# Performance work log

Hardware: AMD Instinct MI355X
Metric: run time of the kernel (lower is better)

The kernel has to match this reference:

```python
import jax, jax.numpy as jnp
import numpy as np

B, N, F = 32, 1024, 7
HID, HID_GLO, MLP_H, OUT = 256, 8, 64, 8
THRESHOLD = 0.3


def setup_inputs() -> dict:
    key = jax.random.key(0)
    ks = jax.random.split(key, 16)
    def lin(k, fan_out, fan_in):
        # xavier-uniform-like init
        lim = (6.0 / (fan_in + fan_out)) ** 0.5
        return jax.random.uniform(k, (fan_out, fan_in), jnp.float32, -lim, lim)
    return {
        "x": jax.random.normal(ks[0], (B, N, F), jnp.float32),
        "W1": lin(ks[1], HID, 2),   "b1": jnp.zeros((HID,), jnp.float32),
        "W2": lin(ks[2], HID, HID), "b2": jnp.zeros((HID,), jnp.float32),
        "Wfc": lin(ks[3], HID, HID), "bfc": jnp.zeros((HID,), jnp.float32),
        "Wg": lin(ks[4], HID_GLO, 2), "bg": jnp.zeros((HID_GLO,), jnp.float32),
        "Wm0": lin(ks[5], MLP_H, N * F), "bm0": jnp.zeros((MLP_H,), jnp.float32),
        "Wm1": lin(ks[6], MLP_H, MLP_H), "bm1": jnp.zeros((MLP_H,), jnp.float32),
        "Wp": lin(ks[7], OUT, MLP_H + HID + HID_GLO), "bp": jnp.zeros((OUT,), jnp.float32),
    }


def reference(x, W1, b1, W2, b2, Wfc, bfc, Wg, bg, Wm0, bm0, Wm1, bm1, Wp, bp):
    # --- GCN branch (torch code detaches node features & adjacency) ---
    pts = jax.lax.stop_gradient(x[:, :, 1:3])                     # [B,N,2]
    diff = pts[:, :, None, :] - pts[:, None, :, :]                # [B,N,N,2]
    dist = jnp.sqrt(jnp.sum(diff * diff, axis=-1))                # [B,N,N]
    adj = (dist < THRESHOLD).astype(x.dtype)                      # [B,N,N]
    dinv = 1.0 / jnp.sqrt(jnp.sum(adj, axis=-1))                  # [B,N] (>=1, self-loop)
    nadj = dinv[:, :, None] * adj * dinv[:, None, :]              # D^-1/2 A D^-1/2
    h = jax.nn.relu(jnp.einsum('bij,bjd->bid', nadj, pts) @ W1.T + b1)   # [B,N,256]
    g = jnp.einsum('bij,bjh->bih', nadj, h) @ W2.T + b2                  # [B,N,256]
    gcn_en = jnp.mean(g, axis=1) @ Wfc.T + bfc                    # [B,256]

    # --- global branch (torch code uses .item() -> constants) ---
    v = jax.lax.stop_gradient(x[:, :, 1:5])                       # [B,N,4]
    avg_speed = jnp.mean(jnp.linalg.norm(v[:, :, 2:4], axis=-1), axis=1)  # [B]
    density = 1.0 / jnp.max(dist, axis=(1, 2))                    # [B] (v3 == pts)
    glo_in = jnp.stack([avg_speed, density], axis=-1)             # [B,2]
    glo_en = jax.nn.relu(glo_in @ Wg.T + bg)                      # [B,8]

    # --- MLP branch on flattened x ---
    xf = x.reshape(x.shape[0], -1)                                # [B, N*F]
    xf = jax.nn.relu(xf @ Wm0.T + bm0)
    xf = jax.nn.relu(xf @ Wm1.T + bm1)                            # [B,64]

    out = jnp.concatenate([xf, gcn_en, glo_en], axis=1) @ Wp.T + bp  # [B,8]
    return out
```

## Files before the change

kernel.cpp:

```cpp
#include <hip/hip_runtime.h>

#define BB 32
#define NN 1024
#define FF 7
#define HID 256
#define MLPH 64
#define OUTN 8
#define CATN (MLPH + HID + 8)

__device__ __forceinline__ float wave_sum(float v) {
#pragma unroll
    for (int m = 32; m >= 1; m >>= 1) v += __shfl_xor(v, m, 64);
    return v;
}
__device__ __forceinline__ float wave_max(float v) {
#pragma unroll
    for (int m = 32; m >= 1; m >>= 1) v = fmaxf(v, __shfl_xor(v, m, 64));
    return v;
}

__global__ __launch_bounds__(1024, 4) void kA(const float* __restrict__ x,
                                              const float* __restrict__ Wm0,
                                              const float* __restrict__ W2,
                                              const float* __restrict__ b2,
                                              const float* __restrict__ Wfc,
                                              const float* __restrict__ bfc,
                                              const float* __restrict__ Wp,
                                              float* __restrict__ deg,
                                              float* __restrict__ bmaxp,
                                              float* __restrict__ spd,
                                              float* __restrict__ mlp_p,
                                              float* __restrict__ E,
                                              float* __restrict__ cE) {
    __shared__ __align__(16) float l0[NN];
    __shared__ __align__(16) float l1[NN];
    __shared__ __align__(16) float s2[NN];
    __shared__ __align__(16) float s3[NN];
    __shared__ float wred[16];
    int blk = blockIdx.x, tid = threadIdx.x, lane = tid & 63, w = tid >> 6;
    if (blk < 256) {
        int b = blk >> 3, jg = blk & 7;
        const float* xb = x + b * (NN * FF);
        l0[tid] = xb[tid * FF + 1];
        l1[tid] = xb[tid * FF + 2];
        __syncthreads();
        int jA = jg * 128 + lane, jB = jA + 64;
        float pj0a = l0[jA], pj1a = l1[jA];
        float pj0b = l0[jB], pj1b = l1[jB];
        const float4* v0p = (const float4*)&l0[w * 64];
        const float4* v1p = (const float4*)&l1[w * 64];
        unsigned dA = 0u, dB = 0u;
        float mx = 0.f;
#pragma unroll 4
        for (int g = 0; g < 16; ++g) {
            float4 v0 = v0p[g], v1 = v1p[g];
            float dx, dy, d2a, d2b;
            dx = pj0a - v0.x; dy = pj1a - v1.x; d2a = fmaf(dy, dy, dx * dx);
            dx = pj0b - v0.x; dy = pj1b - v1.x; d2b = fmaf(dy, dy, dx * dx);
            dA += (d2a <= 0.09f); dB += (d2b <= 0.09f);
            mx = fmaxf(mx, fmaxf(d2a, d2b));
            dx = pj0a - v0.y; dy = pj1a - v1.y; d2a = fmaf(dy, dy, dx * dx);
            dx = pj0b - v0.y; dy = pj1b - v1.y; d2b = fmaf(dy, dy, dx * dx);
            dA += (d2a <= 0.09f); dB += (d2b <= 0.09f);
            mx = fmaxf(mx, fmaxf(d2a, d2b));
            dx = pj0a - v0.z; dy = pj1a - v1.z; d2a = fmaf(dy, dy, dx * dx);
            dx = pj0b - v0.z; dy = pj1b - v1.z; d2b = fmaf(dy, dy, dx * dx);
            dA += (d2a <= 0.09f); dB += (d2b <= 0.09f);
            mx = fmaxf(mx, fmaxf(d2a, d2b));
            dx = pj0a - v0.w; dy = pj1a - v1.w; d2a = fmaf(dy, dy, dx * dx);
            dx = pj0b - v0.w; dy = pj1b - v1.w; d2b = fmaf(dy, dy, dx * dx);
            dA += (d2a <= 0.09f); dB += (d2b <= 0.09f);
            mx = fmaxf(mx, fmaxf(d2a, d2b));
        }
        s2[tid] = (float)dA;
        s3[tid] = (float)dB;
        mx = wave_max(mx);
        if (lane == 0) wred[w] = mx;
        __syncthreads();
        if (tid < 64) {
            float s = 0.f;
#pragma unroll
            for (int kk = 0; kk < 16; ++kk) s += s2[kk * 64 + tid];
            deg[b * NN + jg * 128 + tid] = s;
        } else if (tid < 128) {
            int t = tid - 64;
            float s = 0.f;
#pragma unroll
            for (int kk = 0; kk < 16; ++kk) s += s3[kk * 64 + t];
            deg[b * NN + jg * 128 + 64 + t] = s;
        }
        if (tid == 0) {
            float m = wred[0];
#pragma unroll
            for (int i = 1; i < 16; ++i) m = fmaxf(m, wred[i]);
            bmaxp[b * 8 + jg] = m;
        }
        if (jg == 0) {
            float vx = xb[tid * FF + 3], vy = xb[tid * FF + 4];
            float sp = sqrtf(fmaf(vx, vx, vy * vy));
            sp = wave_sum(sp);
            __syncthreads();
            if (lane == 0) wred[w] = sp;
            __syncthreads();
            if (tid == 0) {
                float s = 0.f;
#pragma unroll
                for (int i = 0; i < 16; ++i) s += wred[i];
                spd[b] = s;
            }
        }
    } else if (blk < 384) {
        int gid = (blk - 256) * 16 + w;
        int b = gid >> 6, h = gid & 63;
        const float4* wr = (const float4*)(Wm0 + h * (NN * FF));
        const float4* xr = (const float4*)(x + b * (NN * FF));
        float4 a4 = {0.f, 0.f, 0.f, 0.f};
#pragma unroll 7
        for (int it = 0; it < 28; ++it) {
            float4 wv = wr[it * 64 + lane];
            float4 xv = xr[it * 64 + lane];
            a4.x = fmaf(wv.x, xv.x, a4.x);
            a4.y = fmaf(wv.y, xv.y, a4.y);
            a4.z = fmaf(wv.z, xv.z, a4.z);
            a4.w = fmaf(wv.w, xv.w, a4.w);
        }
        float s = (a4.x + a4.y) + (a4.z + a4.w);
        s = wave_sum(s);
        if (lane == 0) mlp_p[gid] = s;
    } else {
        int o = blk - 384;
        if (tid < HID) l0[tid] = Wp[o * CATN + MLPH + tid];
        __syncthreads();
        if (tid < HID) {
            float a = 0.f;
#pragma unroll 8
            for (int m = 0; m < HID; ++m) a = fmaf(l0[m], Wfc[m * HID + tid], a);
            l1[tid] = a;
            s2[tid] = l0[tid] * bfc[tid];
        }
        __syncthreads();
        if (tid < HID) {
            float e = 0.f;
#pragma unroll 8
            for (int k = 0; k < HID; ++k) e = fmaf(l1[k], W2[k * HID + tid], e);
            E[o * HID + tid] = e;
            float c = fmaf(l1[tid], b2[tid], s2[tid]);
            c = wave_sum(c);
            if (lane == 0) wred[w] = c;
        }
        __syncthreads();
        if (tid == 0) cE[o] = wred[0] + wred[1] + wred[2] + wred[3];
    }
}

__global__ __launch_bounds__(1024, 4) void kB(const float* __restrict__ x,
                                              const float* __restrict__ deg,
                                              float* __restrict__ q0,
                                              float* __restrict__ q1,
                                              float* __restrict__ wj) {
    __shared__ __align__(16) float l0[NN];
    __shared__ __align__(16) float l1[NN];
    __shared__ __align__(16) float di[NN];
    __shared__ __align__(16) float r0a[NN];
    __shared__ __align__(16) float r1a[NN];
    __shared__ __align__(16) float r2a[NN];
    __shared__ __align__(16) float r0b[NN];
    __shared__ __align__(16) float r1b[NN];
    __shared__ __align__(16) float r2b[NN];
    int blk = blockIdx.x, tid = threadIdx.x, lane = tid & 63, w = tid >> 6;
    int b = blk >> 3, jg = blk & 7;
    const float* xb = x + b * (NN * FF);
    l0[tid] = xb[tid * FF + 1];
    l1[tid] = xb[tid * FF + 2];
    di[tid] = 1.0f / sqrtf(deg[b * NN + tid]);
    __syncthreads();
    int jA = jg * 128 + lane, jB = jA + 64;
    float pj0a = l0[jA], pj1a = l1[jA];
    float pj0b = l0[jB], pj1b = l1[jB];
    const float4* v0p = (const float4*)&l0[w * 64];
    const float4* v1p = (const float4*)&l1[w * 64];
    const float4* vdp = (const float4*)&di[w * 64];
    float a0a = 0.f, a1a = 0.f, asa = 0.f;
    float a0b = 0.f, a1b = 0.f, asb = 0.f;
#pragma unroll 4
    for (int g = 0; g < 16; ++g) {
        float4 v0 = v0p[g], v1 = v1p[g], vd = vdp[g];
        float dx, dy, d2, t;
        dx = pj0a - v0.x; dy = pj1a - v1.x; d2 = fmaf(dy, dy, dx * dx);
        t = (d2 <= 0.09f) ? vd.x : 0.0f;
        a0a = fmaf(t, v0.x, a0a); a1a = fmaf(t, v1.x, a1a); asa += t;
        dx = pj0b - v0.x; dy = pj1b - v1.x; d2 = fmaf(dy, dy, dx * dx);
        t = (d2 <= 0.09f) ? vd.x : 0.0f;
        a0b = fmaf(t, v0.x, a0b); a1b = fmaf(t, v1.x, a1b); asb += t;
        dx = pj0a - v0.y; dy = pj1a - v1.y; d2 = fmaf(dy, dy, dx * dx);
        t = (d2 <= 0.09f) ? vd.y : 0.0f;
        a0a = fmaf(t, v0.y, a0a); a1a = fmaf(t, v1.y, a1a); asa += t;
        dx = pj0b - v0.y; dy = pj1b - v1.y; d2 = fmaf(dy, dy, dx * dx);
        t = (d2 <= 0.09f) ? vd.y : 0.0f;
        a0b = fmaf(t, v0.y, a0b); a1b = fmaf(t, v1.y, a1b); asb += t;
        dx = pj0a - v0.z; dy = pj1a - v1.z; d2 = fmaf(dy, dy, dx * dx);
        t = (d2 <= 0.09f) ? vd.z : 0.0f;
        a0a = fmaf(t, v0.z, a0a); a1a = fmaf(t, v1.z, a1a); asa += t;
        dx = pj0b - v0.z; dy = pj1b - v1.z; d2 = fmaf(dy, dy, dx * dx);
        t = (d2 <= 0.09f) ? vd.z : 0.0f;
        a0b = fmaf(t, v0.z, a0b); a1b = fmaf(t, v1.z, a1b); asb += t;
        dx = pj0a - v0.w; dy = pj1a - v1.w; d2 = fmaf(dy, dy, dx * dx);
        t = (d2 <= 0.09f) ? vd.w : 0.0f;
        a0a = fmaf(t, v0.w, a0a); a1a = fmaf(t, v1.w, a1a); asa += t;
        dx = pj0b - v0.w; dy = pj1b - v1.w; d2 = fmaf(dy, dy, dx * dx);
        t = (d2 <= 0.09f) ? vd.w : 0.0f;
        a0b = fmaf(t, v0.w, a0b); a1b = fmaf(t, v1.w, a1b); asb += t;
    }
    r0a[tid] = a0a; r1a[tid] = a1a; r2a[tid] = asa;
    r0b[tid] = a0b; r1b[tid] = a1b; r2b[tid] = asb;
    __syncthreads();
    if (tid < 128) {
        int t = tid & 63;
        const float* R0 = (tid < 64) ? r0a : r0b;
        const float* R1 = (tid < 64) ? r1a : r1b;
        const float* R2 = (tid < 64) ? r2a : r2b;
        int j = jg * 128 + ((tid < 64) ? 0 : 64) + t;
        float s0 = 0.f, s1 = 0.f, ss = 0.f;
#pragma unroll
        for (int kk = 0; kk < 16; ++kk) {
            s0 += R0[kk * 64 + t];
            s1 += R1[kk * 64 + t];
            ss += R2[kk * 64 + t];
        }
        float dj = di[j];
        q0[b * NN + j] = dj * s0;
        q1[b * NN + j] = dj * s1;
        wj[b * NN + j] = dj * ss * (1.0f / NN);
    }
}

__global__ __launch_bounds__(1024, 4) void kF(const float* __restrict__ q0,
                                              const float* __restrict__ q1,
                                              const float* __restrict__ wj,
                                              const float* __restrict__ W1,
                                              const float* __restrict__ b1,
                                              const float* __restrict__ Wg,
                                              const float* __restrict__ bg,
                                              const float* __restrict__ Wm1,
                                              const float* __restrict__ bm1,
                                              const float* __restrict__ Wp,
                                              const float* __restrict__ bp,
                                              const float* __restrict__ bm0,
                                              const float* __restrict__ mlp_p,
                                              const float* __restrict__ bmaxp,
                                              const float* __restrict__ spd,
                                              const float* __restrict__ E,
                                              const float* __restrict__ cE,
                                              float* __restrict__ out) {
    __shared__ __align__(16) float sq0[NN];
    __shared__ __align__(16) float sq1[NN];
    __shared__ __align__(16) float sw[NN];
    __shared__ __align__(16) float hpp[4][HID];
    __shared__ __align__(16) float hs[HID];
    __shared__ float sx1[MLPH];
    __shared__ float sxf2[MLPH];
    __shared__ float sglo[8];
    int b = blockIdx.x, tid = threadIdx.x;
    sq0[tid] = q0[b * NN + tid];
    sq1[tid] = q1[b * NN + tid];
    sw[tid]  = wj[b * NN + tid];
    if (tid >= 448 && tid < 512) {
        int h = tid - 448;
        sx1[h] = fmaxf(mlp_p[b * MLPH + h] + bm0[h], 0.f);
    }
    __syncthreads();
    {
        int h = tid & 255, jq = tid >> 8;
        float w10 = W1[h * 2], w11 = W1[h * 2 + 1], bb = b1[h];
        float acc = 0.f;
        const float4* q0v4 = (const float4*)&sq0[jq * 256];
        const float4* q1v4 = (const float4*)&sq1[jq * 256];
        const float4* wv4  = (const float4*)&sw[jq * 256];
#pragma unroll 4
        for (int g = 0; g < 64; ++g) {
            float4 q0v = q0v4[g], q1v = q1v4[g], wv = wv4[g];
            acc = fmaf(wv.x, fmaxf(fmaf(q1v.x, w11, fmaf(q0v.x, w10, bb)), 0.f), acc);
            acc = fmaf(wv.y, fmaxf(fmaf(q1v.y, w11, fmaf(q0v.y, w10, bb)), 0.f), acc);
            acc = fmaf(wv.z, fmaxf(fmaf(q1v.z, w11, fmaf(q0v.z, w10, bb)), 0.f), acc);
            acc = fmaf(wv.w, fmaxf(fmaf(q1v.w, w11, fmaf(q0v.w, w10, bb)), 0.f), acc);
        }
        hpp[jq][h] = acc;
    }
    __syncthreads();
    if (tid < HID) {
        hs[tid] = hpp[0][tid] + hpp[1][tid] + hpp[2][tid] + hpp[3][tid];
    } else if (tid < HID + MLPH) {
        int t = tid - HID;
        float a = bm1[t];
        const float* wv = Wm1 + t * MLPH;
#pragma unroll
        for (int k = 0; k < MLPH; ++k) a = fmaf(wv[k], sx1[k], a);
        sxf2[t] = fmaxf(a, 0.f);
    } else if (tid < HID + MLPH + 8) {
        int t = tid - HID - MLPH;
        float mx = 0.f;
#pragma unroll
        for (int g = 0; g < 8; ++g) mx = fmaxf(mx, bmaxp[b * 8 + g]);
        float avg  = spd[b] * (1.0f / NN);
        float dens = 1.0f / sqrtf(mx);
        sglo[t] = fmaxf(fmaf(Wg[t * 2], avg, fmaf(Wg[t * 2 + 1], dens, bg[t])), 0.f);
    }
    __syncthreads();
    if (tid < 512) {
        int o = tid >> 6, lane = tid & 63;
        const float* Eo = E + o * HID;
        float a = Eo[lane] * hs[lane];
        a = fmaf(Eo[lane + 64],  hs[lane + 64],  a);
        a = fmaf(Eo[lane + 128], hs[lane + 128], a);
        a = fmaf(Eo[lane + 192], hs[lane + 192], a);
        a = fmaf(Wp[o * CATN + lane], sxf2[lane], a);
        a = wave_sum(a);
        if (lane == 0) {
            const float* wg = Wp + o * CATN + MLPH + HID;
#pragma unroll
            for (int g = 0; g < 8; ++g) a = fmaf(wg[g], sglo[g], a);
            out[b * OUTN + o] = a + cE[o] + bp[o];
        }
    }
}

extern "C" void kernel_launch(void* const* d_in, const int* in_sizes, int n_in,
                              void* d_out, int out_size, void* d_ws, size_t ws_size,
                              hipStream_t stream) {
    const float* x   = (const float*)d_in[0];
    const float* W1  = (const float*)d_in[1];
    const float* b1  = (const float*)d_in[2];
    const float* W2  = (const float*)d_in[3];
    const float* b2  = (const float*)d_in[4];
    const float* Wfc = (const float*)d_in[5];
    const float* bfc = (const float*)d_in[6];
    const float* Wg  = (const float*)d_in[7];
    const float* bg  = (const float*)d_in[8];
    const float* Wm0 = (const float*)d_in[9];
    const float* bm0 = (const float*)d_in[10];
    const float* Wm1 = (const float*)d_in[11];
    const float* bm1 = (const float*)d_in[12];
    const float* Wp  = (const float*)d_in[13];
    const float* bp  = (const float*)d_in[14];
    float* out = (float*)d_out;
    float* ws  = (float*)d_ws;

    float* deg   = ws;
    float* q0    = ws + 32768;
    float* q1    = ws + 65536;
    float* wj    = ws + 98304;
    float* mlp_p = ws + 131072;
    float* bmaxp = ws + 133120;
    float* spd   = ws + 133376;
    float* E     = ws + 133408;
    float* cE    = ws + 135456;

    kA<<<392, 1024, 0, stream>>>(x, Wm0, W2, b2, Wfc, bfc, Wp,
                                 deg, bmaxp, spd, mlp_p, E, cE);
    kB<<<256, 1024, 0, stream>>>(x, deg, q0, q1, wj);
    kF<<<BB,  1024, 0, stream>>>(q0, q1, wj, W1, b1, Wg, bg, Wm1, bm1, Wp, bp,
                                 bm0, mlp_p, bmaxp, spd, E, cE, out);
}
```

Before: 129.6 us.

## Split prep kernel: extract point coords once, stage Wm0 rows in LDS

Adds a new first kernel that loads each batch's x with coalesced float4 reads, writes the two coordinate columns to contiguous workspace arrays, and computes the speed sum. It also runs the E/cE precompute and the MLP first layer, where each block stages one Wm0 row in LDS and reuses it across all 32 batches. The adjacency and aggregation kernels then read the contiguous coordinates instead of strided x columns. This removes repeated strided gathers and repeated global Wm0 reads, at the cost of an extra kernel launch and a serial dependency before the adjacency pass.

```diff
diff --git a/kernel.cpp b/kernel.cpp
--- a/kernel.cpp
+++ b/kernel.cpp
@@ -19,141 +19,163 @@
     return v;
 }
 
-__global__ __launch_bounds__(1024, 4) void kA(const float* __restrict__ x,
-                                              const float* __restrict__ Wm0,
-                                              const float* __restrict__ W2,
-                                              const float* __restrict__ b2,
-                                              const float* __restrict__ Wfc,
-                                              const float* __restrict__ bfc,
-                                              const float* __restrict__ Wp,
+__global__ __launch_bounds__(1024, 4) void kPM(const float* __restrict__ x,
+                                               const float* __restrict__ Wm0,
+                                               const float* __restrict__ W2,
+                                               const float* __restrict__ b2,
+                                               const float* __restrict__ Wfc,
+                                               const float* __restrict__ bfc,
+                                               const float* __restrict__ Wp,
+                                               float* __restrict__ pts0,
+                                               float* __restrict__ pts1,
+                                               float* __restrict__ spd,
+                                               float* __restrict__ mlp_p,
+                                               float* __restrict__ E,
+                                               float* __restrict__ cE) {
+    __shared__ __align__(16) float sbuf[NN * FF];
+    __shared__ float wred[16];
+    int blk = blockIdx.x, tid = threadIdx.x, lane = tid & 63, w = tid >> 6;
+    if (blk < 32) {
+        int b = blk;
+        const float4* xr = (const float4*)(x + b * (NN * FF));
+        float4* s4 = (float4*)sbuf;
+        for (int i = tid; i < 1792; i += 1024) s4[i] = xr[i];
+        __syncthreads();
+        pts0[b * NN + tid] = sbuf[tid * FF + 1];
+        pts1[b * NN + tid] = sbuf[tid * FF + 2];
+        float vx = sbuf[tid * FF + 3], vy = sbuf[tid * FF + 4];
+        float sp = sqrtf(fmaf(vx, vx, vy * vy));
+        sp = wave_sum(sp);
+        if (lane == 0) wred[w] = sp;
+        __syncthreads();
+        if (tid == 0) {
+            float s = 0.f;
+#pragma unroll
+            for (int i = 0; i < 16; ++i) s += wred[i];
+            spd[b] = s;
+        }
+    } else if (blk < 40) {
+        int o = blk - 32;
+        float* l0 = sbuf;
+        float* l1 = sbuf + 256;
+        float* r2 = sbuf + 512;
+        if (tid < HID) l0[tid] = Wp[o * CATN + MLPH + tid];
+        __syncthreads();
+        if (tid < HID) {
+            float a = 0.f;
+#pragma unroll 8
+            for (int m = 0; m < HID; ++m) a = fmaf(l0[m], Wfc[m * HID + tid], a);
+            l1[tid] = a;
+            r2[tid] = l0[tid] * bfc[tid];
+        }
+        __syncthreads();
+        if (tid < HID) {
+            float e = 0.f;
+#pragma unroll 8
+            for (int k = 0; k < HID; ++k) e = fmaf(l1[k], W2[k * HID + tid], e);
+            E[o * HID + tid] = e;
+            float c = fmaf(l1[tid], b2[tid], r2[tid]);
+            c = wave_sum(c);
+            if (lane == 0) wred[w] = c;
+        }
+        __syncthreads();
+        if (tid == 0) cE[o] = wred[0] + wred[1] + wred[2] + wred[3];
+    } else {
+        int h = blk - 40;
+        const float4* wr = (const float4*)(Wm0 + h * (NN * FF));
+        float4* s4 = (float4*)sbuf;
+        for (int i = tid; i < 1792; i += 1024) s4[i] = wr[i];
+        __syncthreads();
+#pragma unroll
+        for (int rep = 0; rep < 2; ++rep) {
+            int b = w * 2 + rep;
+            const float4* xr = (const float4*)(x + b * (NN * FF));
+            float4 a4 = {0.f, 0.f, 0.f, 0.f};
+#pragma unroll 7
+            for (int it = 0; it < 28; ++it) {
+                float4 xv = xr[it * 64 + lane];
+                float4 wv = s4[it * 64 + lane];
+                a4.x = fmaf(wv.x, xv.x, a4.x);
+                a4.y = fmaf(wv.y, xv.y, a4.y);
+                a4.z = fmaf(wv.z, xv.z, a4.z);
+                a4.w = fmaf(wv.w, xv.w, a4.w);
+            }
+            float s = (a4.x + a4.y) + (a4.z + a4.w);
+            s = wave_sum(s);
+            if (lane == 0) mlp_p[b * MLPH + h] = s;
+        }
+    }
+}
+
+__global__ __launch_bounds__(1024, 4) void kA(const float* __restrict__ pts0,
+                                              const float* __restrict__ pts1,
                                               float* __restrict__ deg,
-                                              float* __restrict__ bmaxp,
-                                              float* __restrict__ spd,
-                                              float* __restrict__ mlp_p,
-                                              float* __restrict__ E,
-                                              float* __restrict__ cE) {
+                                              float* __restrict__ bmaxp) {
     __shared__ __align__(16) float l0[NN];
     __shared__ __align__(16) float l1[NN];
     __shared__ __align__(16) float s2[NN];
     __shared__ __align__(16) float s3[NN];
     __shared__ float wred[16];
     int blk = blockIdx.x, tid = threadIdx.x, lane = tid & 63, w = tid >> 6;
-    if (blk < 256) {
-        int b = blk >> 3, jg = blk & 7;
-        const float* xb = x + b * (NN * FF);
-        l0[tid] = xb[tid * FF + 1];
-        l1[tid] = xb[tid * FF + 2];
-        __syncthreads();
-        int jA = jg * 128 + lane, jB = jA + 64;
-        float pj0a = l0[jA], pj1a = l1[jA];
-        float pj0b = l0[jB], pj1b = l1[jB];
-        const float4* v0p = (const float4*)&l0[w * 64];
-        const float4* v1p = (const float4*)&l1[w * 64];
-        unsigned dA = 0u, dB = 0u;
-        float mx = 0.f;
+    int b = blk >> 3, jg = blk & 7;
+    l0[tid] = pts0[b * NN + tid];
+    l1[tid] = pts1[b * NN + tid];
+    __syncthreads();
+    int jA = jg * 128 + lane, jB = jA + 64;
+    float pj0a = l0[jA], pj1a = l1[jA];
+    float pj0b = l0[jB], pj1b = l1[jB];
+    const float4* v0p = (const float4*)&l0[w * 64];
+    const float4* v1p = (const float4*)&l1[w * 64];
+    unsigned dA = 0u, dB = 0u;
+    float mx = 0.f;
 #pragma unroll 4
-        for (int g = 0; g < 16; ++g) {
-            float4 v0 = v0p[g], v1 = v1p[g];
-            float dx, dy, d2a, d2b;
-            dx = pj0a - v0.x; dy = pj1a - v1.x; d2a = fmaf(dy, dy, dx * dx);
-            dx = pj0b - v0.x; dy = pj1b - v1.x; d2b = fmaf(dy, dy, dx * dx);
-            dA += (d2a <= 0.09f); dB += (d2b <= 0.09f);
-            mx = fmaxf(mx, fmaxf(d2a, d2b));
-            dx = pj0a - v0.y; dy = pj1a - v1.y; d2a = fmaf(dy, dy, dx * dx);
-            dx = pj0b - v0.y; dy = pj1b - v1.y; d2b = fmaf(dy, dy, dx * dx);
-            dA += (d2a <= 0.09f); dB += (d2b <= 0.09f);
-            mx = fmaxf(mx, fmaxf(d2a, d2b));
-            dx = pj0a - v0.z; dy = pj1a - v1.z; d2a = fmaf(dy, dy, dx * dx);
-            dx = pj0b - v0.z; dy = pj1b - v1.z; d2b = fmaf(dy, dy, dx * dx);
-            dA += (d2a <= 0.09f); dB += (d2b <= 0.09f);
-            mx = fmaxf(mx, fmaxf(d2a, d2b));
-            dx = pj0a - v0.w; dy = pj1a - v1.w; d2a = fmaf(dy, dy, dx * dx);
-            dx = pj0b - v0.w; dy = pj1b - v1.w; d2b = fmaf(dy, dy, dx * dx);
-            dA += (d2a <= 0.09f); dB += (d2b <= 0.09f);
-            mx = fmaxf(mx, fmaxf(d2a, d2b));
-        }
-        s2[tid] = (float)dA;
-        s3[tid] = (float)dB;
-        mx = wave_max(mx);
-        if (lane == 0) wred[w] = mx;
-        __syncthreads();
-        if (tid < 64) {
-            float s = 0.f;
-#pragma unroll
-            for (int kk = 0; kk < 16; ++kk) s += s2[kk * 64 + tid];
-            deg[b * NN + jg * 128 + tid] = s;
-        } else if (tid < 128) {
-            int t = tid - 64;
-            float s = 0.f;
-#pragma unroll
-            for (int kk = 0; kk < 16; ++kk) s += s3[kk * 64 + t];
-            deg[b * NN + jg * 128 + 64 + t] = s;
-        }
-        if (tid == 0) {
-            float m = wred[0];
-#pragma unroll
-            for (int i = 1; i < 16; ++i) m = fmaxf(m, wred[i]);
-            bmaxp[b * 8 + jg] = m;
-        }
-        if (jg == 0) {
-            float vx = xb[tid * FF + 3], vy = xb[tid * FF + 4];
-            float sp = sqrtf(fmaf(vx, vx, vy * vy));
-            sp = wave_sum(sp);
-            __syncthreads();
-            if (lane == 0) wred[w] = sp;
-            __syncthreads();
-            if (tid == 0) {
-                float s = 0.f;
-#pragma unroll
-                for (int i = 0; i < 16; ++i) s += wred[i];
-                spd[b] = s;
-            }
-        }
-    } else if (blk < 384) {
-        int gid = (blk - 256) * 16 + w;
-        int b = gid >> 6, h = gid & 63;
-        const float4* wr = (const float4*)(Wm0 + h * (NN * FF));
-        const float4* xr = (const float4*)(x + b * (NN * FF));
-        float4 a4 = {0.f, 0.f, 0.f, 0.f};
-#pragma unroll 7
-        for (int it = 0; it < 28; ++it) {
-            float4 wv = wr[it * 64 + lane];
-            float4 xv = xr[it * 64 + lane];
-            a4.x = fmaf(wv.x, xv.x, a4.x);
-            a4.y = fmaf(wv.y, xv.y, a4.y);
-            a4.z = fmaf(wv.z, xv.z, a4.z);
-            a4.w = fmaf(wv.w, xv.w, a4.w);
-        }
-        float s = (a4.x + a4.y) + (a4.z + a4.w);
-        s = wave_sum(s);
-        if (lane == 0) mlp_p[gid] = s;
-    } else {
-        int o = blk - 384;
-        if (tid < HID) l0[tid] = Wp[o * CATN + MLPH + tid];
-        __syncthreads();
-        if (tid < HID) {
-            float a = 0.f;
-#pragma unroll 8
-            for (int m = 0; m < HID; ++m) a = fmaf(l0[m], Wfc[m * HID + tid], a);
-            l1[tid] = a;
-            s2[tid] = l0[tid] * bfc[tid];
-        }
-        __syncthreads();
-        if (tid < HID) {
-            float e = 0.f;
-#pragma unroll 8
-            for (int k = 0; k < HID; ++k) e = fmaf(l1[k], W2[k * HID + tid], e);
-            E[o * HID + tid] = e;
-            float c = fmaf(l1[tid], b2[tid], s2[tid]);
-            c = wave_sum(c);
-            if (lane == 0) wred[w] = c;
-        }
-        __syncthreads();
-        if (tid == 0) cE[o] = wred[0] + wred[1] + wred[2] + wred[3];
-    }
-}
-
-__global__ __launch_bounds__(1024, 4) void kB(const float* __restrict__ x,
+    for (int g = 0; g < 16; ++g) {
+        float4 v0 = v0p[g], v1 = v1p[g];
+        float dx, dy, d2a, d2b;
+        dx = pj0a - v0.x; dy = pj1a - v1.x; d2a = fmaf(dy, dy, dx * dx);
+        dx = pj0b - v0.x; dy = pj1b - v1.x; d2b = fmaf(dy, dy, dx * dx);
+        dA += (d2a <= 0.09f); dB += (d2b <= 0.09f);
+        mx = fmaxf(mx, fmaxf(d2a, d2b));
+        dx = pj0a - v0.y; dy = pj1a - v1.y; d2a = fmaf(dy, dy, dx * dx);
+        dx = pj0b - v0.y; dy = pj1b - v1.y; d2b = fmaf(dy, dy, dx * dx);
+        dA += (d2a <= 0.09f); dB += (d2b <= 0.09f);
+        mx = fmaxf(mx, fmaxf(d2a, d2b));
+        dx = pj0a - v0.z; dy = pj1a - v1.z; d2a = fmaf(dy, dy, dx * dx);
+        dx = pj0b - v0.z; dy = pj1b - v1.z; d2b = fmaf(dy, dy, dx * dx);
+        dA += (d2a <= 0.09f); dB += (d2b <= 0.09f);
+        mx = fmaxf(mx, fmaxf(d2a, d2b));
+        dx = pj0a - v0.w; dy = pj1a - v1.w; d2a = fmaf(dy, dy, dx * dx);
+        dx = pj0b - v0.w; dy = pj1b - v1.w; d2b = fmaf(dy, dy, dx * dx);
+        dA += (d2a <= 0.09f); dB += (d2b <= 0.09f);
+        mx = fmaxf(mx, fmaxf(d2a, d2b));
+    }
+    s2[tid] = (float)dA;
+    s3[tid] = (float)dB;
+    mx = wave_max(mx);
+    if (lane == 0) wred[w] = mx;
+    __syncthreads();
+    if (tid < 64) {
+        float s = 0.f;
+#pragma unroll
+        for (int kk = 0; kk < 16; ++kk) s += s2[kk * 64 + tid];
+        deg[b * NN + jg * 128 + tid] = s;
+    } else if (tid < 128) {
+        int t = tid - 64;
+        float s = 0.f;
+#pragma unroll
+        for (int kk = 0; kk < 16; ++kk) s += s3[kk * 64 + t];
+        deg[b * NN + jg * 128 + 64 + t] = s;
+    }
+    if (tid == 0) {
+        float m = wred[0];
+#pragma unroll
+        for (int i = 1; i < 16; ++i) m = fmaxf(m, wred[i]);
+        bmaxp[b * 8 + jg] = m;
+    }
+}
+
+__global__ __launch_bounds__(1024, 4) void kB(const float* __restrict__ pts0,
+                                              const float* __restrict__ pts1,
                                               const float* __restrict__ deg,
                                               float* __restrict__ q0,
                                               float* __restrict__ q1,
@@ -169,9 +191,8 @@
     __shared__ __align__(16) float r2b[NN];
     int blk = blockIdx.x, tid = threadIdx.x, lane = tid & 63, w = tid >> 6;
     int b = blk >> 3, jg = blk & 7;
-    const float* xb = x + b * (NN * FF);
-    l0[tid] = xb[tid * FF + 1];
-    l1[tid] = xb[tid * FF + 2];
+    l0[tid] = pts0[b * NN + tid];
+    l1[tid] = pts1[b * NN + tid];
     di[tid] = 1.0f / sqrtf(deg[b * NN + tid]);
     __syncthreads();
     int jA = jg * 128 + lane, jB = jA + 64;
@@ -345,19 +366,22 @@
     float* out = (float*)d_out;
     float* ws  = (float*)d_ws;
 
-    float* deg   = ws;
-    float* q0    = ws + 32768;
-    float* q1    = ws + 65536;
-    float* wj    = ws + 98304;
-    float* mlp_p = ws + 131072;
-    float* bmaxp = ws + 133120;
-    float* spd   = ws + 133376;
-    float* E     = ws + 133408;
-    float* cE    = ws + 135456;
-
-    kA<<<392, 1024, 0, stream>>>(x, Wm0, W2, b2, Wfc, bfc, Wp,
-                                 deg, bmaxp, spd, mlp_p, E, cE);
-    kB<<<256, 1024, 0, stream>>>(x, deg, q0, q1, wj);
-    kF<<<BB,  1024, 0, stream>>>(q0, q1, wj, W1, b1, Wg, bg, Wm1, bm1, Wp, bp,
-                                 bm0, mlp_p, bmaxp, spd, E, cE, out);
-}
+    float* pts0  = ws;
+    float* pts1  = ws + 32768;
+    float* deg   = ws + 65536;
+    float* q0    = ws + 98304;
+    float* q1    = ws + 131072;
+    float* wj    = ws + 163840;
+    float* mlp_p = ws + 196608;
+    float* bmaxp = ws + 198656;
+    float* spd   = ws + 198912;
+    float* E     = ws + 198944;
+    float* cE    = ws + 200992;
+
+    kPM<<<104, 1024, 0, stream>>>(x, Wm0, W2, b2, Wfc, bfc, Wp,
+                                  pts0, pts1, spd, mlp_p, E, cE);
+    kA<<<256,  1024, 0, stream>>>(pts0, pts1, deg, bmaxp);
+    kB<<<256,  1024, 0, stream>>>(pts0, pts1, deg, q0, q1, wj);
+    kF<<<BB,   1024, 0, stream>>>(q0, q1, wj, W1, b1, Wg, bg, Wm1, bm1, Wp, bp,
+                                  bm0, mlp_p, bmaxp, spd, E, cE, out);
+}
```

Measured after the change: 128.7 us (median of 2 runs). About the same (-0.7%).

## Fuse final GCN/MLP kernel into aggregation kernel with last-block atomic reduction

Applied to the files above, without the earlier changes.

Merges the third kernel into the second one. Each of the 8 blocks per batch now computes its partial hidden-feature sums from its own 128 nodes. An atomic counter elects the last block per batch, which reduces the partials and writes the output. The MLP layer-0 blocks now stage one Wm0 row in shared memory and reuse it across all 32 batches, instead of re-reading weights per batch. This removes a kernel launch and the q0/q1/wj round trip through memory. In exchange it adds threadfence/atomic synchronization and a larger shared-memory footprint, which lowers occupancy.

```diff
diff --git a/kernel.cpp b/kernel.cpp
--- a/kernel.cpp
+++ b/kernel.cpp
@@ -19,26 +19,28 @@
     return v;
 }
 
-__global__ __launch_bounds__(1024, 4) void kA(const float* __restrict__ x,
-                                              const float* __restrict__ Wm0,
-                                              const float* __restrict__ W2,
-                                              const float* __restrict__ b2,
-                                              const float* __restrict__ Wfc,
-                                              const float* __restrict__ bfc,
-                                              const float* __restrict__ Wp,
-                                              float* __restrict__ deg,
-                                              float* __restrict__ bmaxp,
-                                              float* __restrict__ spd,
-                                              float* __restrict__ mlp_p,
-                                              float* __restrict__ E,
-                                              float* __restrict__ cE) {
-    __shared__ __align__(16) float l0[NN];
-    __shared__ __align__(16) float l1[NN];
-    __shared__ __align__(16) float s2[NN];
-    __shared__ __align__(16) float s3[NN];
+__global__ __launch_bounds__(1024, 2) void kD1(const float* __restrict__ x,
+                                               const float* __restrict__ Wm0,
+                                               const float* __restrict__ W2,
+                                               const float* __restrict__ b2,
+                                               const float* __restrict__ Wfc,
+                                               const float* __restrict__ bfc,
+                                               const float* __restrict__ Wp,
+                                               float* __restrict__ deg,
+                                               float* __restrict__ bmaxp,
+                                               float* __restrict__ spd,
+                                               float* __restrict__ mlp_p,
+                                               float* __restrict__ E,
+                                               float* __restrict__ cE,
+                                               unsigned* __restrict__ cnt) {
+    __shared__ __align__(16) float sbuf[NN * FF];
     __shared__ float wred[16];
     int blk = blockIdx.x, tid = threadIdx.x, lane = tid & 63, w = tid >> 6;
     if (blk < 256) {
+        float* l0 = sbuf;
+        float* l1 = sbuf + NN;
+        float* s2 = sbuf + 2 * NN;
+        float* s3 = sbuf + 3 * NN;
         int b = blk >> 3, jg = blk & 7;
         const float* xb = x + b * (NN * FF);
         l0[tid] = xb[tid * FF + 1];
@@ -107,28 +109,38 @@
 #pragma unroll
                 for (int i = 0; i < 16; ++i) s += wred[i];
                 spd[b] = s;
+                cnt[b] = 0u;
             }
         }
-    } else if (blk < 384) {
-        int gid = (blk - 256) * 16 + w;
-        int b = gid >> 6, h = gid & 63;
+    } else if (blk < 320) {
+        int h = blk - 256;
         const float4* wr = (const float4*)(Wm0 + h * (NN * FF));
-        const float4* xr = (const float4*)(x + b * (NN * FF));
-        float4 a4 = {0.f, 0.f, 0.f, 0.f};
+        float4* s4 = (float4*)sbuf;
+        for (int i = tid; i < 1792; i += 1024) s4[i] = wr[i];
+        __syncthreads();
+#pragma unroll
+        for (int rep = 0; rep < 2; ++rep) {
+            int b = w * 2 + rep;
+            const float4* xr = (const float4*)(x + b * (NN * FF));
+            float4 a4 = {0.f, 0.f, 0.f, 0.f};
 #pragma unroll 7
-        for (int it = 0; it < 28; ++it) {
-            float4 wv = wr[it * 64 + lane];
-            float4 xv = xr[it * 64 + lane];
-            a4.x = fmaf(wv.x, xv.x, a4.x);
-            a4.y = fmaf(wv.y, xv.y, a4.y);
-            a4.z = fmaf(wv.z, xv.z, a4.z);
-            a4.w = fmaf(wv.w, xv.w, a4.w);
-        }
-        float s = (a4.x + a4.y) + (a4.z + a4.w);
-        s = wave_sum(s);
-        if (lane == 0) mlp_p[gid] = s;
+            for (int it = 0; it < 28; ++it) {
+                float4 xv = xr[it * 64 + lane];
+                float4 wv = s4[it * 64 + lane];
+                a4.x = fmaf(wv.x, xv.x, a4.x);
+                a4.y = fmaf(wv.y, xv.y, a4.y);
+                a4.z = fmaf(wv.z, xv.z, a4.z);
+                a4.w = fmaf(wv.w, xv.w, a4.w);
+            }
+            float s = (a4.x + a4.y) + (a4.z + a4.w);
+            s = wave_sum(s);
+            if (lane == 0) mlp_p[b * MLPH + h] = s;
+        }
     } else {
-        int o = blk - 384;
+        int o = blk - 320;
+        float* l0 = sbuf;
+        float* l1 = sbuf + 256;
+        float* r2 = sbuf + 512;
         if (tid < HID) l0[tid] = Wp[o * CATN + MLPH + tid];
         __syncthreads();
         if (tid < HID) {
@@ -136,7 +148,7 @@
 #pragma unroll 8
             for (int m = 0; m < HID; ++m) a = fmaf(l0[m], Wfc[m * HID + tid], a);
             l1[tid] = a;
-            s2[tid] = l0[tid] * bfc[tid];
+            r2[tid] = l0[tid] * bfc[tid];
         }
         __syncthreads();
         if (tid < HID) {
@@ -144,7 +156,7 @@
 #pragma unroll 8
             for (int k = 0; k < HID; ++k) e = fmaf(l1[k], W2[k * HID + tid], e);
             E[o * HID + tid] = e;
-            float c = fmaf(l1[tid], b2[tid], s2[tid]);
+            float c = fmaf(l1[tid], b2[tid], r2[tid]);
             c = wave_sum(c);
             if (lane == 0) wred[w] = c;
         }
@@ -153,11 +165,27 @@
     }
 }
 
-__global__ __launch_bounds__(1024, 4) void kB(const float* __restrict__ x,
-                                              const float* __restrict__ deg,
-                                              float* __restrict__ q0,
-                                              float* __restrict__ q1,
-                                              float* __restrict__ wj) {
+__global__ __launch_bounds__(1024, 2) void kD2(const float* __restrict__ x,
+                                               const float* __restrict__ deg,
+                                               const float* __restrict__ W1,
+                                               const float* __restrict__ b1,
+                                               const float* __restrict__ Wg,
+                                               const float* __restrict__ bg,
+                                               const float* __restrict__ Wm1,
+                                               const float* __restrict__ bm1,
+                                               const float* __restrict__ Wp,
+                                               const float* __restrict__ bp,
+                                               const float* __restrict__ bm0,
+                                               const float* __restrict__ mlp_p,
+                                               const float* __restrict__ bmaxp,
+                                               const float* __restrict__ spd,
+                                               const float* __restrict__ E,
+                                               const float* __restrict__ cE,
+                                               float* __restrict__ hp,
+                                               float* __restrict__ xf2g,
+                                               float* __restrict__ sglog,
+                                               unsigned* __restrict__ cnt,
+                                               float* __restrict__ out) {
     __shared__ __align__(16) float l0[NN];
     __shared__ __align__(16) float l1[NN];
     __shared__ __align__(16) float di[NN];
@@ -167,6 +195,11 @@
     __shared__ __align__(16) float r0b[NN];
     __shared__ __align__(16) float r1b[NN];
     __shared__ __align__(16) float r2b[NN];
+    __shared__ __align__(16) float sq0[128];
+    __shared__ __align__(16) float sq1[128];
+    __shared__ __align__(16) float swj[128];
+    __shared__ __align__(16) float hpp[4][HID];
+    __shared__ unsigned s_old;
     int blk = blockIdx.x, tid = threadIdx.x, lane = tid & 63, w = tid >> 6;
     int b = blk >> 3, jg = blk & 7;
     const float* xb = x + b * (NN * FF);
@@ -219,7 +252,7 @@
         const float* R0 = (tid < 64) ? r0a : r0b;
         const float* R1 = (tid < 64) ? r1a : r1b;
         const float* R2 = (tid < 64) ? r2a : r2b;
-        int j = jg * 128 + ((tid < 64) ? 0 : 64) + t;
+        int jl = ((tid < 64) ? 0 : 64) + t;
         float s0 = 0.f, s1 = 0.f, ss = 0.f;
 #pragma unroll
         for (int kk = 0; kk < 16; ++kk) {
@@ -227,99 +260,80 @@
             s1 += R1[kk * 64 + t];
             ss += R2[kk * 64 + t];
         }
-        float dj = di[j];
-        q0[b * NN + j] = dj * s0;
-        q1[b * NN + j] = dj * s1;
-        wj[b * NN + j] = dj * ss * (1.0f / NN);
-    }
-}
-
-__global__ __launch_bounds__(1024, 4) void kF(const float* __restrict__ q0,
-                                              const float* __restrict__ q1,
-                                              const float* __restrict__ wj,
-                                              const float* __restrict__ W1,
-                                              const float* __restrict__ b1,
-                                              const float* __restrict__ Wg,
-                                              const float* __restrict__ bg,
-                                              const float* __restrict__ Wm1,
-                                              const float* __restrict__ bm1,
-                                              const float* __restrict__ Wp,
-                                              const float* __restrict__ bp,
-                                              const float* __restrict__ bm0,
-                                              const float* __restrict__ mlp_p,
-                                              const float* __restrict__ bmaxp,
-                                              const float* __restrict__ spd,
-                                              const float* __restrict__ E,
-                                              const float* __restrict__ cE,
-                                              float* __restrict__ out) {
-    __shared__ __align__(16) float sq0[NN];
-    __shared__ __align__(16) float sq1[NN];
-    __shared__ __align__(16) float sw[NN];
-    __shared__ __align__(16) float hpp[4][HID];
-    __shared__ __align__(16) float hs[HID];
-    __shared__ float sx1[MLPH];
-    __shared__ float sxf2[MLPH];
-    __shared__ float sglo[8];
-    int b = blockIdx.x, tid = threadIdx.x;
-    sq0[tid] = q0[b * NN + tid];
-    sq1[tid] = q1[b * NN + tid];
-    sw[tid]  = wj[b * NN + tid];
-    if (tid >= 448 && tid < 512) {
-        int h = tid - 448;
-        sx1[h] = fmaxf(mlp_p[b * MLPH + h] + bm0[h], 0.f);
+        float dj = di[jg * 128 + jl];
+        sq0[jl] = dj * s0;
+        sq1[jl] = dj * s1;
+        swj[jl] = dj * ss * (1.0f / NN);
     }
     __syncthreads();
     {
         int h = tid & 255, jq = tid >> 8;
         float w10 = W1[h * 2], w11 = W1[h * 2 + 1], bb = b1[h];
         float acc = 0.f;
-        const float4* q0v4 = (const float4*)&sq0[jq * 256];
-        const float4* q1v4 = (const float4*)&sq1[jq * 256];
-        const float4* wv4  = (const float4*)&sw[jq * 256];
-#pragma unroll 4
-        for (int g = 0; g < 64; ++g) {
-            float4 q0v = q0v4[g], q1v = q1v4[g], wv = wv4[g];
-            acc = fmaf(wv.x, fmaxf(fmaf(q1v.x, w11, fmaf(q0v.x, w10, bb)), 0.f), acc);
-            acc = fmaf(wv.y, fmaxf(fmaf(q1v.y, w11, fmaf(q0v.y, w10, bb)), 0.f), acc);
-            acc = fmaf(wv.z, fmaxf(fmaf(q1v.z, w11, fmaf(q0v.z, w10, bb)), 0.f), acc);
-            acc = fmaf(wv.w, fmaxf(fmaf(q1v.w, w11, fmaf(q0v.w, w10, bb)), 0.f), acc);
+        const float* q0v = &sq0[jq * 32];
+        const float* q1v = &sq1[jq * 32];
+        const float* wv  = &swj[jq * 32];
+#pragma unroll 8
+        for (int i = 0; i < 32; ++i) {
+            float t = fmaf(q1v[i], w11, fmaf(q0v[i], w10, bb));
+            acc = fmaf(wv[i], fmaxf(t, 0.f), acc);
         }
         hpp[jq][h] = acc;
     }
     __syncthreads();
-    if (tid < HID) {
-        hs[tid] = hpp[0][tid] + hpp[1][tid] + hpp[2][tid] + hpp[3][tid];
-    } else if (tid < HID + MLPH) {
-        int t = tid - HID;
-        float a = bm1[t];
-        const float* wv = Wm1 + t * MLPH;
-#pragma unroll
-        for (int k = 0; k < MLPH; ++k) a = fmaf(wv[k], sx1[k], a);
-        sxf2[t] = fmaxf(a, 0.f);
-    } else if (tid < HID + MLPH + 8) {
-        int t = tid - HID - MLPH;
+    if (tid < HID)
+        hp[(b * 8 + jg) * HID + tid] =
+            hpp[0][tid] + hpp[1][tid] + hpp[2][tid] + hpp[3][tid];
+    if (jg == 1 && tid < MLPH) {
+        r0a[tid] = fmaxf(mlp_p[b * MLPH + tid] + bm0[tid], 0.f);
+    }
+    if (jg == 1) __syncthreads();
+    if (jg == 1 && tid < MLPH) {
+        float a = bm1[tid];
+        const float* wv = Wm1 + tid * MLPH;
+#pragma unroll
+        for (int k = 0; k < MLPH; ++k) a = fmaf(wv[k], r0a[k], a);
+        xf2g[b * MLPH + tid] = fmaxf(a, 0.f);
+    }
+    if (jg == 2 && tid < 8) {
         float mx = 0.f;
 #pragma unroll
         for (int g = 0; g < 8; ++g) mx = fmaxf(mx, bmaxp[b * 8 + g]);
         float avg  = spd[b] * (1.0f / NN);
         float dens = 1.0f / sqrtf(mx);
-        sglo[t] = fmaxf(fmaf(Wg[t * 2], avg, fmaf(Wg[t * 2 + 1], dens, bg[t])), 0.f);
-    }
-    __syncthreads();
-    if (tid < 512) {
-        int o = tid >> 6, lane = tid & 63;
-        const float* Eo = E + o * HID;
-        float a = Eo[lane] * hs[lane];
-        a = fmaf(Eo[lane + 64],  hs[lane + 64],  a);
-        a = fmaf(Eo[lane + 128], hs[lane + 128], a);
-        a = fmaf(Eo[lane + 192], hs[lane + 192], a);
-        a = fmaf(Wp[o * CATN + lane], sxf2[lane], a);
-        a = wave_sum(a);
-        if (lane == 0) {
-            const float* wg = Wp + o * CATN + MLPH + HID;
-#pragma unroll
-            for (int g = 0; g < 8; ++g) a = fmaf(wg[g], sglo[g], a);
-            out[b * OUTN + o] = a + cE[o] + bp[o];
+        sglog[b * 8 + tid] =
+            fmaxf(fmaf(Wg[tid * 2], avg, fmaf(Wg[tid * 2 + 1], dens, bg[tid])), 0.f);
+    }
+    __syncthreads();
+    __threadfence();
+    if (tid == 0) s_old = atomicAdd(&cnt[b], 1u);
+    __syncthreads();
+    if (s_old == 7u) {
+        __threadfence();
+        if (tid < HID) {
+            float s = 0.f;
+#pragma unroll
+            for (int g = 0; g < 8; ++g) s += hp[(b * 8 + g) * HID + tid];
+            r1a[tid] = s;
+        }
+        if (tid >= 512 && tid < 576) r2a[tid - 512] = xf2g[b * MLPH + (tid - 512)];
+        if (tid >= 576 && tid < 584) r2b[tid - 576] = sglog[b * 8 + (tid - 576)];
+        __syncthreads();
+        if (tid < 512) {
+            int o = tid >> 6;
+            const float* Eo = E + o * HID;
+            float a = Eo[lane] * r1a[lane];
+            a = fmaf(Eo[lane + 64],  r1a[lane + 64],  a);
+            a = fmaf(Eo[lane + 128], r1a[lane + 128], a);
+            a = fmaf(Eo[lane + 192], r1a[lane + 192], a);
+            a = fmaf(Wp[o * CATN + lane], r2a[lane], a);
+            a = wave_sum(a);
+            if (lane == 0) {
+                const float* wg = Wp + o * CATN + MLPH + HID;
+#pragma unroll
+                for (int g = 0; g < 8; ++g) a = fmaf(wg[g], r2b[g], a);
+                out[b * OUTN + o] = a + cE[o] + bp[o];
+            }
         }
     }
 }
@@ -345,19 +359,20 @@
     float* out = (float*)d_out;
     float* ws  = (float*)d_ws;
 
-    float* deg   = ws;
-    float* q0    = ws + 32768;
-    float* q1    = ws + 65536;
-    float* wj    = ws + 98304;
-    float* mlp_p = ws + 131072;
-    float* bmaxp = ws + 133120;
-    float* spd   = ws + 133376;
-    float* E     = ws + 133408;
-    float* cE    = ws + 135456;
-
-    kA<<<392, 1024, 0, stream>>>(x, Wm0, W2, b2, Wfc, bfc, Wp,
-                                 deg, bmaxp, spd, mlp_p, E, cE);
-    kB<<<256, 1024, 0, stream>>>(x, deg, q0, q1, wj);
-    kF<<<BB,  1024, 0, stream>>>(q0, q1, wj, W1, b1, Wg, bg, Wm1, bm1, Wp, bp,
-                                 bm0, mlp_p, bmaxp, spd, E, cE, out);
-}
+    float*    deg   = ws;
+    float*    mlp_p = ws + 32768;
+    float*    bmaxp = ws + 34816;
+    float*    spd   = ws + 35072;
+    float*    E     = ws + 35104;
+    float*    cE    = ws + 37152;
+    float*    hp    = ws + 37160;
+    float*    xf2g  = ws + 102696;
+    float*    sglog = ws + 104744;
+    unsigned* cnt   = (unsigned*)(ws + 105000);
+
+    kD1<<<328, 1024, 0, stream>>>(x, Wm0, W2, b2, Wfc, bfc, Wp,
+                                  deg, bmaxp, spd, mlp_p, E, cE, cnt);
+    kD2<<<256, 1024, 0, stream>>>(x, deg, W1, b1, Wg, bg, Wm1, bm1, Wp, bp,
+                                  bm0, mlp_p, bmaxp, spd, E, cE,
+                                  hp, xf2g, sglog, cnt, out);
+}
```

New measurement: 216.9 us. +67.3%, slower.
